# Optimization experiments

Measured on AMD Instinct MI355X. Metric: run time of the kernel, lower is better.

## Reference

```python
import jax, jax.numpy as jnp
import numpy as np

BN_EPS = 1e-5
VQ_TEMP = 0.1

B, K, D_AUDIO, D_TEXT, VOCAB = 256, 8, 768, 512, 49408


def setup_inputs() -> dict:
    key = jax.random.key(0)
    k1, k2, k3, k4, k5 = jax.random.split(key, 5)
    return {
        "audio_kw": jax.random.normal(k1, (B, K, D_AUDIO), dtype=jnp.float32),
        "W_proj": jax.random.normal(k2, (D_AUDIO, D_TEXT), dtype=jnp.float32) * 0.02,
        "b_proj": jnp.zeros((D_TEXT,), dtype=jnp.float32),
        "bn_gamma": jax.random.uniform(k3, (D_TEXT,), dtype=jnp.float32, minval=0.5, maxval=1.5),
        "bn_beta": jax.random.normal(k4, (D_TEXT,), dtype=jnp.float32) * 0.01,
        "emb": jax.random.normal(k5, (VOCAB, D_TEXT), dtype=jnp.float32) * 0.02,
    }


def reference(audio_kw, W_proj, b_proj, bn_gamma, bn_beta, emb):
    # keyword projection: [B,K,Da] @ [Da,Dt] -> [B,K,Dt]
    proj = jnp.einsum("bkd,de->bke", audio_kw, W_proj) + b_proj
    # Kw_BatchNorm: batchnorm over (batch, keyword) per text feature, affine
    mean = jnp.mean(proj, axis=(0, 1))
    var = jnp.var(proj, axis=(0, 1))
    bn = (proj - mean) * jax.lax.rsqrt(var + BN_EPS) * bn_gamma + bn_beta
    # cosine similarity against full vocab table (one fused normalize+GEMM,
    # equivalent to the per-keyword F.cosine_similarity loop in the original)
    bn_n = bn / jnp.linalg.norm(bn, axis=-1, keepdims=True)
    emb_n = emb / jnp.linalg.norm(emb, axis=-1, keepdims=True)
    cos_score = jnp.einsum("bke,ve->bkv", bn_n, emb_n)  # [B,K,V]
    # VQ: temperature softmax over the vocab, then soft lookup
    subword_prob = jax.nn.softmax(cos_score / VQ_TEMP, axis=-1)
    vq_keywords = jnp.einsum("bkv,ve->bke", subword_prob, emb)  # [B,K,Dt]
    return vq_keywords
```

## Files before the change

### kernel.cpp

```cpp
#include <hip/hip_runtime.h>
#include <stdint.h>

typedef unsigned short u16;
typedef _Float16 f16;
typedef __attribute__((ext_vector_type(8))) _Float16 f16x8;
typedef __attribute__((ext_vector_type(4))) float f32x4;

#define DA 768
#define DT 512
#define NV 49408
#define MTOT 2048
#define NB_N 193
#define KS 16

__device__ __forceinline__ u16 f2h(float f) {
  return __builtin_bit_cast(u16, (f16)f);
}
__device__ __forceinline__ float h2f(u16 u) {
  return (float)__builtin_bit_cast(f16, u);
}

__device__ __forceinline__ void gload16(const void* g, void* l) {
  __builtin_amdgcn_global_load_lds((const __attribute__((address_space(1))) void*)g,
                                   (__attribute__((address_space(3))) void*)l,
                                   16, 0, 0);
}
#define SBAR()   __builtin_amdgcn_s_barrier()
#define SCHED0() __builtin_amdgcn_sched_barrier(0)
#define MFMA16(a, b, c) __builtin_amdgcn_mfma_f32_16x16x32_f16((a), (b), (c), 0, 0, 0)

__global__ __launch_bounds__(256) void k_a2h(const float* __restrict__ a,
                                             u16* __restrict__ ah) {
  int i = (blockIdx.x * 256 + threadIdx.x) * 8;
  float4 x = *(const float4*)&a[i];
  float4 y = *(const float4*)&a[i + 4];
  union { u16 u[8]; int4 q; } pk;
  pk.u[0] = f2h(x.x); pk.u[1] = f2h(x.y); pk.u[2] = f2h(x.z); pk.u[3] = f2h(x.w);
  pk.u[4] = f2h(y.x); pk.u[5] = f2h(y.y); pk.u[6] = f2h(y.z); pk.u[7] = f2h(y.w);
  *(int4*)&ah[i] = pk.q;
}

__global__ __launch_bounds__(256) void k_wT(const float* __restrict__ W,
                                            u16* __restrict__ WT) {
  __shared__ float tile[64][65];
  const int k0 = blockIdx.y * 64, n0 = blockIdx.x * 64;
  const int t = threadIdx.x;
  const int r = t >> 4, c4 = (t & 15) * 4;
#pragma unroll
  for (int i = 0; i < 4; ++i) {
    float4 x = *(const float4*)&W[(size_t)(k0 + r + i * 16) * DT + n0 + c4];
    tile[r + i * 16][c4 + 0] = x.x; tile[r + i * 16][c4 + 1] = x.y;
    tile[r + i * 16][c4 + 2] = x.z; tile[r + i * 16][c4 + 3] = x.w;
  }
  __syncthreads();
  const int nr = t >> 2, kc = (t & 3) * 16;
  union { u16 u[8]; int4 q; } p0, p1;
#pragma unroll
  for (int i = 0; i < 8; ++i) p0.u[i] = f2h(tile[kc + i][nr]);
#pragma unroll
  for (int i = 0; i < 8; ++i) p1.u[i] = f2h(tile[kc + 8 + i][nr]);
  u16* dst = WT + (size_t)(n0 + nr) * DA + k0 + kc;
  *(int4*)dst = p0.q;
  *(int4*)(dst + 8) = p1.q;
}

__global__ __launch_bounds__(256) void k_stats(const float* __restrict__ P,
                                               float* __restrict__ pstat) {
  const int t = threadIdx.x;
  const int r0 = blockIdx.x * 32;
  float s0 = 0, q0 = 0, s1 = 0, q1 = 0;
  for (int r = r0; r < r0 + 32; ++r) {
    float x0 = P[(size_t)r * DT + t];
    float x1 = P[(size_t)r * DT + t + 256];
    s0 += x0; q0 += x0 * x0; s1 += x1; q1 += x1 * x1;
  }
  float* d = pstat + (size_t)blockIdx.x * 1024;
  d[t] = s0; d[t + 256] = s1; d[512 + t] = q0; d[768 + t] = q1;
}

__global__ __launch_bounds__(256) void k_stats2(const float* __restrict__ pstat,
                                                float* __restrict__ stats) {
  int c = blockIdx.x * 256 + threadIdx.x;
  float s = 0.f;
  for (int b = 0; b < 64; ++b) s += pstat[(size_t)b * 1024 + c];
  stats[c] = s;
}

__global__ __launch_bounds__(64) void k_bnnorm(const float* __restrict__ P,
                                               const float* __restrict__ stats,
                                               const float* __restrict__ gamma,
                                               const float* __restrict__ beta,
                                               u16* __restrict__ bnn) {
  const int r = blockIdx.x, l = threadIdx.x;
  float v[8];
  float ss = 0.f;
#pragma unroll
  for (int i = 0; i < 8; ++i) {
    int c = l * 8 + i;
    float mean = stats[c] * (1.f / MTOT);
    float var = stats[DT + c] * (1.f / MTOT) - mean * mean;
    float is = rsqrtf(var + 1e-5f);
    float x = (P[(size_t)r * DT + c] - mean) * is * gamma[c] + beta[c];
    v[i] = x; ss += x * x;
  }
#pragma unroll
  for (int off = 32; off > 0; off >>= 1) ss += __shfl_xor(ss, off);
  float rn = rsqrtf(ss);
  union { u16 u[8]; int4 q; } pk;
#pragma unroll
  for (int i = 0; i < 8; ++i) pk.u[i] = f2h(v[i] * rn);
  *(int4*)&bnn[(size_t)r * DT + l * 8] = pk.q;
}

__global__ __launch_bounds__(256) void k_embprep2(const float* __restrict__ emb,
                                                  u16* __restrict__ embH,
                                                  u16* __restrict__ embT,
                                                  float* __restrict__ invn) {
  __shared__ float tile[64][65];
  const int v0 = blockIdx.x * 64;
  const int t = threadIdx.x;
  const int r = t >> 4, c4 = (t & 15) * 4;
  const int vr = t >> 2, hc = (t & 3) * 16;
  const int dr = t >> 2, vc = (t & 3) * 16;
  float ssq = 0.f;
  for (int d0 = 0; d0 < DT; d0 += 64) {
    __syncthreads();
#pragma unroll
    for (int i = 0; i < 4; ++i) {
      float4 x = *(const float4*)&emb[(size_t)(v0 + r + i * 16) * DT + d0 + c4];
      tile[r + i * 16][c4 + 0] = x.x; tile[r + i * 16][c4 + 1] = x.y;
      tile[r + i * 16][c4 + 2] = x.z; tile[r + i * 16][c4 + 3] = x.w;
    }
    __syncthreads();
    union { u16 u[8]; int4 q; } pa, pb;
#pragma unroll
    for (int i = 0; i < 8; ++i) { float f = tile[vr][hc + i];     pa.u[i] = f2h(f); ssq += f * f; }
#pragma unroll
    for (int i = 0; i < 8; ++i) { float f = tile[vr][hc + 8 + i]; pb.u[i] = f2h(f); ssq += f * f; }
    *(int4*)&embH[(size_t)(v0 + vr) * DT + d0 + hc] = pa.q;
    *(int4*)&embH[(size_t)(v0 + vr) * DT + d0 + hc + 8] = pb.q;
    union { u16 u[8]; int4 q; } p0, p1;
#pragma unroll
    for (int i = 0; i < 8; ++i) p0.u[i] = f2h(tile[vc + i][dr]);
#pragma unroll
    for (int i = 0; i < 8; ++i) p1.u[i] = f2h(tile[vc + 8 + i][dr]);
    u16* dst = embT + (size_t)(d0 + dr) * NV + v0 + vc;
    *(int4*)dst = p0.q;
    *(int4*)(dst + 8) = p1.q;
  }
  ssq += __shfl_xor(ssq, 1);
  ssq += __shfl_xor(ssq, 2);
  if ((t & 3) == 0) invn[v0 + vr] = rsqrtf(ssq) * 10.0f;
}

__device__ __forceinline__ void kloop256(const f16* __restrict__ A,
                                         const f16* __restrict__ B,
                                         int lda, int ldb, size_t kb, int NT,
                                         int m0, int n0, int tid,
                                         f16* ldsA, f16* ldsB,
                                         f32x4 (&acc)[4][4]) {
  const int l = tid & 63, lr = l & 15, lg = l >> 4;
  const int w = tid >> 6, wm = w >> 2, wn = w & 3;
  const int rA = tid >> 2, qA = tid & 3;
  const int qsA = qA ^ ((rA >> 1) & 3);
  const f16* gA = A + (size_t)(m0 + rA) * lda + kb + qsA * 8;
  const f16* gB0;
  const f16* gB1;
  { int r = tid >> 2, q = tid & 3; int qs = q ^ ((r >> 1) & 3);
    gB0 = B + (size_t)(n0 + r) * ldb + kb + qs * 8; }
  { int c = tid + 512; int r = c >> 2, q = c & 3; int qs = q ^ ((r >> 1) & 3);
    gB1 = B + (size_t)(n0 + r) * ldb + kb + qs * 8; }
  auto STAGE = [&](int buf, int k0) {
    gload16(gA + k0, (void*)&ldsA[(size_t)buf * 4096 + (size_t)tid * 8]);
    gload16(gB0 + k0, (void*)&ldsB[(size_t)buf * 8192 + (size_t)tid * 8]);
    gload16(gB1 + k0, (void*)&ldsB[(size_t)buf * 8192 + (size_t)(tid + 512) * 8]);
  };
  const int gsw = lg ^ ((lr >> 1) & 3);

  STAGE(0, 0);
  STAGE(1, 32);
  asm volatile("s_waitcnt vmcnt(3)" ::: "memory"); SCHED0();
  SBAR(); SCHED0();
  int cur = 0;
  for (int it = 0; it < NT; ++it) {
    const f16* bufA = ldsA + cur * 4096;
    const f16* bufB = ldsB + cur * 8192;
    f16x8 af[4], bf[4];
#pragma unroll
    for (int i = 0; i < 4; ++i)
      af[i] = *(const f16x8*)&bufA[(wm * 64 + i * 16 + lr) * 32 + gsw * 8];
#pragma unroll
    for (int j = 0; j < 4; ++j)
      bf[j] = *(const f16x8*)&bufB[(wn * 64 + j * 16 + lr) * 32 + gsw * 8];
#pragma unroll
    for (int i = 0; i < 4; ++i)
#pragma unroll
      for (int j = 0; j < 4; ++j)
        acc[i][j] = MFMA16(af[i], bf[j], acc[i][j]);
    asm volatile("s_waitcnt lgkmcnt(0)" ::: "memory"); SCHED0();
    SBAR(); SCHED0();
    if (it + 2 < NT) {
      STAGE(cur, (it + 2) * 32);
      asm volatile("s_waitcnt vmcnt(3)" ::: "memory");
    } else {
      asm volatile("s_waitcnt vmcnt(0)" ::: "memory");
    }
    SCHED0();
    SBAR(); SCHED0();
    cur ^= 1;
  }
}

__global__ __launch_bounds__(512) void k_proj(const f16* __restrict__ A,
                                              const f16* __restrict__ Bt,
                                              const float* __restrict__ bias,
                                              float* __restrict__ P) {
  __shared__ f16 sm[24576];
  const int t = threadIdx.x;
  const int l = t & 63, lr = l & 15, lg = l >> 4;
  const int w = t >> 6, wm = w >> 2, wn = w & 3;
  const int m0 = blockIdx.x * 128;
  const int n0 = blockIdx.y * 256;

  f32x4 acc[4][4];
#pragma unroll
  for (int i = 0; i < 4; ++i)
#pragma unroll
    for (int j = 0; j < 4; ++j) acc[i][j] = (f32x4){0.f, 0.f, 0.f, 0.f};

  kloop256(A, Bt, DA, DA, 0, DA / 32, m0, n0, t, sm, sm + 8192, acc);

#pragma unroll
  for (int j = 0; j < 4; ++j) {
    int col = n0 + wn * 64 + j * 16 + lr;
    float bj = bias[col];
#pragma unroll
    for (int i = 0; i < 4; ++i)
#pragma unroll
      for (int rg = 0; rg < 4; ++rg) {
        int row = m0 + wm * 64 + i * 16 + lg * 4 + rg;
        P[(size_t)row * DT + col] = acc[i][j][rg] + bj;
      }
  }
}

__global__ __launch_bounds__(512) void k_score(const f16* __restrict__ A,
                                               const f16* __restrict__ Bt,
                                               const float* __restrict__ invn,
                                               u16* __restrict__ E,
                                               float* __restrict__ lpart,
                                               int row0, int CH) {
  __shared__ f16 sm[24576];
  __shared__ float psum[512];
  const int t = threadIdx.x;
  const int l = t & 63, lr = l & 15, lg = l >> 4;
  const int w = t >> 6, wm = w >> 2, wn = w & 3;
  const int mB = CH >> 7;
  const int nwg = NB_N * mB;
  const int o = blockIdx.x + blockIdx.y * NB_N;
  const int v = (o & 7) * (nwg >> 3) + (o >> 3);
  const int nb = v / mB, by = v % mB;
  const int n0 = nb * 256;
  const int mloc = by * 128;
  const int m0 = row0 + mloc;

  f32x4 acc[4][4];
#pragma unroll
  for (int i = 0; i < 4; ++i)
#pragma unroll
    for (int j = 0; j < 4; ++j) acc[i][j] = (f32x4){0.f, 0.f, 0.f, 0.f};

  kloop256(A, Bt, DT, DT, 0, DT / 32, m0, n0, t, sm, sm + 8192, acc);

  float inv_j[4];
#pragma unroll
  for (int j = 0; j < 4; ++j) inv_j[j] = invn[n0 + wn * 64 + j * 16 + lr];
  float rs[4][4] = {};
#pragma unroll
  for (int r2 = 0; r2 < 2; ++r2) {
    if (wm == r2) {
#pragma unroll
      for (int i = 0; i < 4; ++i)
#pragma unroll
        for (int j = 0; j < 4; ++j)
#pragma unroll
          for (int rg = 0; rg < 4; ++rg) {
            float e = __expf(acc[i][j][rg] * inv_j[j]);
            rs[i][rg] += e;
            int lrow = i * 16 + lg * 4 + rg;
            sm[lrow * 256 + wn * 64 + j * 16 + lr] = (f16)e;
          }
    }
    __syncthreads();
#pragma unroll
    for (int cc = 0; cc < 4; ++cc) {
      int chunk = t + cc * 512;
      int row = chunk >> 5, g = chunk & 31;
      *(int4*)&E[(size_t)(mloc + r2 * 64 + row) * NV + n0 + g * 8] =
          *(const int4*)&sm[chunk * 8];
    }
    __syncthreads();
  }
#pragma unroll
  for (int m = 1; m <= 8; m <<= 1)
#pragma unroll
    for (int i = 0; i < 4; ++i)
#pragma unroll
      for (int rg = 0; rg < 4; ++rg) rs[i][rg] += __shfl_xor(rs[i][rg], m);
  if (lr == 0) {
#pragma unroll
    for (int i = 0; i < 4; ++i)
#pragma unroll
      for (int rg = 0; rg < 4; ++rg)
        psum[(wm * 64 + i * 16 + lg * 4 + rg) * 4 + wn] = rs[i][rg];
  }
  __syncthreads();
  if (t < 128)
    lpart[(size_t)nb * CH + mloc + t] =
        psum[t * 4 + 0] + psum[t * 4 + 1] + psum[t * 4 + 2] + psum[t * 4 + 3];
}

__global__ __launch_bounds__(512) void k_pv(const f16* __restrict__ A,
                                            const f16* __restrict__ Bt,
                                            u16* __restrict__ Op,
                                            int CH) {
  __shared__ f16 sm[24576];
  const int t = threadIdx.x;
  const int l = t & 63, lr = l & 15, lg = l >> 4;
  const int w = t >> 6, wm = w >> 2, wn = w & 3;
  const int mB = CH >> 7;
  const int nwg = 2 * mB * KS;
  const int o = blockIdx.x + blockIdx.y * 2 + blockIdx.z * 2 * mB;
  const int v = (o & 7) * (nwg >> 3) + (o >> 3);
  const int n = v & 1;
  const int m = (v >> 1) % mB;
  const int z = v / (2 * mB);
  const int n0 = n * 256;
  const int m0 = m * 128;
  const int g0 = z * 96 + (z < 8 ? z : 8);
  const int NT = 96 + (z < 8 ? 1 : 0);
  const size_t kb = (size_t)g0 * 32;

  f32x4 acc[4][4];
#pragma unroll
  for (int i = 0; i < 4; ++i)
#pragma unroll
    for (int j = 0; j < 4; ++j) acc[i][j] = (f32x4){0.f, 0.f, 0.f, 0.f};

  kloop256(A, Bt, NV, NV, kb, NT, m0, n0, t, sm, sm + 8192, acc);

#pragma unroll
  for (int i = 0; i < 4; ++i)
#pragma unroll
    for (int j = 0; j < 4; ++j)
#pragma unroll
      for (int rg = 0; rg < 4; ++rg) {
        int row = m0 + wm * 64 + i * 16 + lg * 4 + rg;
        int col = n0 + wn * 64 + j * 16 + lr;
        Op[((size_t)z * CH + row) * DT + col] = f2h(acc[i][j][rg]);
      }
}

__global__ __launch_bounds__(256) void k_lred(const float* __restrict__ lp,
                                              float* __restrict__ lv, int CH) {
  int rb = blockIdx.x * 256 + threadIdx.x;
  float s = 0.f;
  for (int nb = 0; nb < NB_N; ++nb) s += lp[(size_t)nb * CH + rb];
  lv[rb] = s;
}

__global__ __launch_bounds__(256) void k_out(const u16* __restrict__ Op,
                                             const float* __restrict__ lv,
                                             float* __restrict__ out,
                                             int row0, int CH) {
  int idx = blockIdx.x * 256 + threadIdx.x;
  int rb = idx >> 9, c = idx & 511;
  float s = 0.f;
#pragma unroll
  for (int zz = 0; zz < KS; ++zz) s += h2f(Op[((size_t)zz * CH + rb) * DT + c]);
  out[(size_t)(row0 + rb) * DT + c] = s / lv[rb];
}

extern "C" void kernel_launch(void* const* d_in, const int* in_sizes, int n_in,
                              void* d_out, int out_size, void* d_ws, size_t ws_size,
                              hipStream_t stream) {
  const float* audio = (const float*)d_in[0];
  const float* W     = (const float*)d_in[1];
  const float* bias  = (const float*)d_in[2];
  const float* gamma = (const float*)d_in[3];
  const float* beta  = (const float*)d_in[4];
  const float* emb   = (const float*)d_in[5];
  float* out = (float*)d_out;

  char* ws = (char*)d_ws;
  size_t off = 0;
  auto alloc = [&](size_t bytes) {
    char* p = ws + off;
    off += (bytes + 255) & ~(size_t)255;
    return p;
  };
  float* proj   = (float*)alloc((size_t)MTOT * DT * 4);
  float* pstat  = (float*)alloc((size_t)64 * 1024 * 4);
  float* stats  = (float*)alloc((size_t)2 * DT * 4);
  u16*   bnnH   = (u16*)alloc((size_t)MTOT * DT * 2);
  u16*   embH   = (u16*)alloc((size_t)NV * DT * 2);
  u16*   embT   = (u16*)alloc((size_t)DT * NV * 2);
  float* invn   = (float*)alloc((size_t)NV * 4);
  u16*   audioH = (u16*)alloc((size_t)MTOT * DA * 2);
  u16*   WT     = (u16*)alloc((size_t)DT * DA * 2);
  size_t fixed_off = off;

  int CH = 2048;
  while (CH > 256) {
    size_t need = fixed_off;
    need += (((size_t)CH * NV * 2) + 255) & ~(size_t)255;
    need += (((size_t)NB_N * CH * 4) + 255) & ~(size_t)255;
    need += (((size_t)CH * 4) + 255) & ~(size_t)255;
    need += (((size_t)KS * CH * DT * 2) + 255) & ~(size_t)255;
    if (need <= ws_size) break;
    CH >>= 1;
  }
  u16*   E     = (u16*)alloc((size_t)CH * NV * 2);
  float* lpart = (float*)alloc((size_t)NB_N * CH * 4);
  float* lvec  = (float*)alloc((size_t)CH * 4);
  u16*   Op    = (u16*)alloc((size_t)KS * CH * DT * 2);
  if (ws_size < off) return;

  k_a2h<<<dim3(MTOT * DA / 2048), dim3(256), 0, stream>>>(audio, audioH);
  k_wT<<<dim3(DT / 64, DA / 64), dim3(256), 0, stream>>>(W, WT);
  k_proj<<<dim3(MTOT / 128, 2), dim3(512), 0, stream>>>(
      (const f16*)audioH, (const f16*)WT, bias, proj);
  k_stats<<<dim3(64), dim3(256), 0, stream>>>(proj, pstat);
  k_stats2<<<dim3(4), dim3(256), 0, stream>>>(pstat, stats);
  k_bnnorm<<<dim3(MTOT), dim3(64), 0, stream>>>(proj, stats, gamma, beta, bnnH);
  k_embprep2<<<dim3(NV / 64), dim3(256), 0, stream>>>(emb, embH, embT, invn);

  for (int row0 = 0; row0 < MTOT; row0 += CH) {
    k_score<<<dim3(NB_N, CH / 128), dim3(512), 0, stream>>>(
        (const f16*)bnnH, (const f16*)embH, invn, E, lpart, row0, CH);
    k_lred<<<dim3(CH / 256), dim3(256), 0, stream>>>(lpart, lvec, CH);
    k_pv<<<dim3(2, CH / 128, KS), dim3(512), 0, stream>>>(
        (const f16*)E, (const f16*)embT, Op, CH);
    k_out<<<dim3(CH * 2), dim3(256), 0, stream>>>(Op, lvec, out, row0, CH);
  }
}
```

Measured before the change: 402.5 us.

## Enlarge k_pv tile to 256x256 with 1024 threads and inline double-buffered loop

The P·V split-K GEMM kernel now uses 1024-thread workgroups covering a 256x256 output tile instead of 128x256, with 64KB of dynamic LDS holding double-buffered A and B stages. The shared kloop256 helper is replaced by an inline pipeline that issues direct global-to-LDS loads two stages ahead with XOR-swizzled layout. The intent is to reuse each B tile across twice as many rows, cutting global traffic for the embedding table and improving MFMA density. The cost is half as many workgroups, heavier register and LDS pressure, and possibly lower occupancy.

```diff
diff --git a/kernel.cpp b/kernel.cpp
--- a/kernel.cpp
+++ b/kernel.cpp
@@ -320,15 +320,17 @@
         psum[t * 4 + 0] + psum[t * 4 + 1] + psum[t * 4 + 2] + psum[t * 4 + 3];
 }
 
-__global__ __launch_bounds__(512) void k_pv(const f16* __restrict__ A,
-                                            const f16* __restrict__ Bt,
-                                            u16* __restrict__ Op,
-                                            int CH) {
-  __shared__ f16 sm[24576];
+__global__ __launch_bounds__(1024) void k_pv(const f16* __restrict__ A,
+                                             const f16* __restrict__ Bt,
+                                             u16* __restrict__ Op,
+                                             int CH) {
+  extern __shared__ char lds[];
+  f16* ldsA = (f16*)lds;
+  f16* ldsB = (f16*)(lds + 32768);
   const int t = threadIdx.x;
   const int l = t & 63, lr = l & 15, lg = l >> 4;
   const int w = t >> 6, wm = w >> 2, wn = w & 3;
-  const int mB = CH >> 7;
+  const int mB = CH >> 8;
   const int nwg = 2 * mB * KS;
   const int o = blockIdx.x + blockIdx.y * 2 + blockIdx.z * 2 * mB;
   const int v = (o & 7) * (nwg >> 3) + (o >> 3);
@@ -336,18 +338,60 @@
   const int m = (v >> 1) % mB;
   const int z = v / (2 * mB);
   const int n0 = n * 256;
-  const int m0 = m * 128;
+  const int m0 = m * 256;
   const int g0 = z * 96 + (z < 8 ? z : 8);
   const int NT = 96 + (z < 8 ? 1 : 0);
   const size_t kb = (size_t)g0 * 32;
 
+  const int rS = t >> 2, qS = t & 3;
+  const int qsS = qS ^ ((rS >> 1) & 3);
+  const f16* gA = A + (size_t)(m0 + rS) * NV + kb + qsS * 8;
+  const f16* gB = Bt + (size_t)(n0 + rS) * NV + kb + qsS * 8;
+  auto STAGE = [&](int buf, int kt) {
+    int k0 = kt * 32;
+    gload16(gA + k0, (void*)&ldsA[(size_t)buf * 8192 + (size_t)t * 8]);
+    gload16(gB + k0, (void*)&ldsB[(size_t)buf * 8192 + (size_t)t * 8]);
+  };
+  const int gsw = lg ^ ((lr >> 1) & 3);
+
   f32x4 acc[4][4];
 #pragma unroll
   for (int i = 0; i < 4; ++i)
 #pragma unroll
     for (int j = 0; j < 4; ++j) acc[i][j] = (f32x4){0.f, 0.f, 0.f, 0.f};
 
-  kloop256(A, Bt, NV, NV, kb, NT, m0, n0, t, sm, sm + 8192, acc);
+  STAGE(0, 0);
+  STAGE(1, 1);
+  asm volatile("s_waitcnt vmcnt(2)" ::: "memory"); SCHED0();
+  SBAR(); SCHED0();
+  int cur = 0;
+  for (int it = 0; it < NT; ++it) {
+    const f16* bufA = ldsA + cur * 8192;
+    const f16* bufB = ldsB + cur * 8192;
+    f16x8 af[4], bf[4];
+#pragma unroll
+    for (int i = 0; i < 4; ++i)
+      af[i] = *(const f16x8*)&bufA[(wm * 64 + i * 16 + lr) * 32 + gsw * 8];
+#pragma unroll
+    for (int j = 0; j < 4; ++j)
+      bf[j] = *(const f16x8*)&bufB[(wn * 64 + j * 16 + lr) * 32 + gsw * 8];
+#pragma unroll
+    for (int i = 0; i < 4; ++i)
+#pragma unroll
+      for (int j = 0; j < 4; ++j)
+        acc[i][j] = MFMA16(af[i], bf[j], acc[i][j]);
+    asm volatile("s_waitcnt lgkmcnt(0)" ::: "memory"); SCHED0();
+    SBAR(); SCHED0();
+    if (it + 2 < NT) {
+      STAGE(cur, it + 2);
+      asm volatile("s_waitcnt vmcnt(2)" ::: "memory");
+    } else {
+      asm volatile("s_waitcnt vmcnt(0)" ::: "memory");
+    }
+    SCHED0();
+    SBAR(); SCHED0();
+    cur ^= 1;
+  }
 
 #pragma unroll
   for (int i = 0; i < 4; ++i)
@@ -426,6 +470,9 @@
   u16*   Op    = (u16*)alloc((size_t)KS * CH * DT * 2);
   if (ws_size < off) return;
 
+  hipFuncSetAttribute((const void*)k_pv,
+                      hipFuncAttributeMaxDynamicSharedMemorySize, 65536);
+
   k_a2h<<<dim3(MTOT * DA / 2048), dim3(256), 0, stream>>>(audio, audioH);
   k_wT<<<dim3(DT / 64, DA / 64), dim3(256), 0, stream>>>(W, WT);
   k_proj<<<dim3(MTOT / 128, 2), dim3(512), 0, stream>>>(
@@ -439,7 +486,7 @@
     k_score<<<dim3(NB_N, CH / 128), dim3(512), 0, stream>>>(
         (const f16*)bnnH, (const f16*)embH, invn, E, lpart, row0, CH);
     k_lred<<<dim3(CH / 256), dim3(256), 0, stream>>>(lpart, lvec, CH);
-    k_pv<<<dim3(2, CH / 128, KS), dim3(512), 0, stream>>>(
+    k_pv<<<dim3(2, CH >> 8, KS), dim3(1024), 65536, stream>>>(
         (const f16*)E, (const f16*)embT, Op, CH);
     k_out<<<dim3(CH * 2), dim3(256), 0, stream>>>(Op, lvec, out, row0, CH);
   }
```

Result: faster. 391.7 us (median of 2 runs) (-2.7%).
